# Performance work log

Measured on AMD Instinct MI355X. Metric: run time of the kernel, lower is better.

## Reference

```python
import jax, jax.numpy as jnp
import numpy as np
from jax import lax

DEPTH = 8
LEAK = 0.01  # activations.relu(x, 0.01) == leaky relu


def _lrelu(z):
    return jnp.where(z >= 0, z, LEAK * z)


def _forward(x, mask, bucket_size, W_emb, b_emb, W, U, b, W1, b1,
             W_action_1, U_action_1, b_action_1, W_action_3, b_action_3):
    S = int(bucket_size)
    B = x.shape[0]
    H = W_emb.shape[1]
    dm = mask.T[:S]                         # [S,B] data mask (float)
    xe = x @ W_emb + b_emb                  # [B,S,H] embedding
    xe = jnp.transpose(xe, (1, 0, 2))[:S]   # [S,B,H] time-major
    # last_value_mask: 1 only at the final time step
    lvm = jnp.concatenate([jnp.zeros((S - 1, B), jnp.float32),
                           jnp.ones((1, B), jnp.float32)], axis=0)

    def hstep(carry, seq):
        h_tm1, nm_tm1, hv_tm1 = carry
        xt, pm, phv, lv = seq
        # action MLP -> per-sample gate
        a = _lrelu(xt @ W_action_1 + h_tm1 @ U_action_1 + b_action_1)  # [B,A]
        nm = jnp.clip(0.2 * (a @ W_action_3 + b_action_3) + 0.5, 0.0, 1.0)[:, 0]  # hard_sigmoid
        nm = (1.0 - lv) * (pm * phv * nm)
        both = pm * phv * (1.0 - nm) * hv_tm1
        x_only = pm * phv * (nm + (1.0 - nm) * (1.0 - hv_tm1))
        h_only = (1.0 - pm + pm * (1.0 - phv)) * (1.0 - nm) * hv_tm1
        hv = both + x_only + h_only
        h_ = _lrelu(xt @ W + h_tm1 @ U + b)      # [B,inner]
        h_ = _lrelu(h_ @ W1 + b1)                # [B,H]
        h = both[:, None] * h_ + x_only[:, None] * xt + h_only[:, None] * h_tm1
        return (h, nm, hv), (h, nm, hv)

    def vstep(carry, _):
        xv, xm, phv = carry  # [S,B,H], [S,B], [S,B]
        init = (jnp.zeros((B, H), jnp.float32),
                jnp.ones((B,), jnp.float32),
                jnp.zeros((B,), jnp.float32))
        _, (hs, nms, hvs) = lax.scan(hstep, init, (xv, xm, phv, lvm))
        # shift new_mask left by one step, pad last step with ones
        nms = jnp.concatenate([nms[1:], jnp.ones((1, B), jnp.float32)], axis=0)
        return (hs, nms, hvs), None

    (hfin, _, _), _ = lax.scan(vstep, (xe, dm, dm), None, length=DEPTH - 1)
    return hfin[-1]  # [B,H]: last time step of the last vertical level


def setup_inputs() -> dict:
    key = jax.random.key(0)
    ks = jax.random.split(key, 9)
    B, S, IN, H, INNER, A = 64, 256, 256, 256, 512, 64
    g = lambda k, shp: jax.random.normal(k, shp, jnp.float32) * np.float32(np.sqrt(2.0 / (shp[0] + shp[1])))
    return {
        "x": jax.random.normal(ks[0], (B, S, IN), jnp.float32),
        "mask": jnp.ones((B, S), jnp.float32),
        "bucket_size": S,
        "W_emb": g(ks[1], (IN, H)),
        "b_emb": jnp.zeros((H,), jnp.float32),
        "W": g(ks[2], (H, INNER)),
        "U": g(ks[3], (H, INNER)),
        "b": jnp.zeros((INNER,), jnp.float32),
        "W1": g(ks[4], (INNER, H)),
        "b1": jnp.zeros((H,), jnp.float32),
        "W_action_1": g(ks[5], (H, A)),
        "U_action_1": g(ks[6], (H, A)),
        "b_action_1": jnp.zeros((A,), jnp.float32),
        "W_action_3": g(ks[7], (A, 1)),
        "b_action_3": jnp.zeros((1,), jnp.float32),
    }


def reference(x, mask, bucket_size, W_emb, b_emb, W, U, b, W1, b1,
              W_action_1, U_action_1, b_action_1, W_action_3, b_action_3):
    return _forward(x, mask, bucket_size, W_emb, b_emb, W, U, b, W1, b1,
                    W_action_1, U_action_1, b_action_1, W_action_3, b_action_3)
```

## Files before the change

### kernel.cpp

```cpp
#include <hip/hip_runtime.h>
#include <stdint.h>


typedef _Float16 f16x8 __attribute__((ext_vector_type(8)));
typedef float    f32x4 __attribute__((ext_vector_type(4)));

static constexpr int SS = 256, BB = 64, DIN = 256, DH = 256, DNN = 512, DA = 64;

static constexpr size_t OFF_FLAGS = 0;
static constexpr size_t OFF_WEMB  = 8192;
static constexpr size_t SZ_WEMB   = (size_t)DIN * DH * 2;
static constexpr size_t OFF_W     = OFF_WEMB + SZ_WEMB;
static constexpr size_t SZ_WU     = (size_t)DH * DNN * 2;
static constexpr size_t OFF_U     = OFF_W + SZ_WU;
static constexpr size_t OFF_W1    = OFF_U + SZ_WU;
static constexpr size_t SZ_W1     = (size_t)DNN * DH * 2;
static constexpr size_t OFF_WA1   = OFF_W1 + SZ_W1;
static constexpr size_t SZ_WA     = (size_t)DH * DA * 2;
static constexpr size_t OFF_UA1   = OFF_WA1 + SZ_WA;
static constexpr size_t OFF_NM    = OFF_UA1 + SZ_WA;
static constexpr size_t SZ_NM     = (size_t)SS * BB * 4;
static constexpr size_t OFF_HV    = OFF_NM + 8 * SZ_NM;
static constexpr size_t OFF_G1    = OFF_HV + 8 * SZ_NM;
static constexpr size_t SZ_G1     = (size_t)BB * DNN * 2;
static constexpr size_t OFF_Z     = OFF_G1 + 8 * SZ_G1;
static constexpr size_t OFF_HB    = (size_t)4 << 20;
static constexpr size_t SZ_HB     = (size_t)SS * BB * DH * 2;
static constexpr size_t WS_NEEDED = OFF_HB + 8 * SZ_HB;

__device__ __forceinline__ float lrelu(float v) { return v >= 0.0f ? v : 0.01f * v; }

__device__ __forceinline__ float gldf(const float* p) {
  return __hip_atomic_load((float*)p, __ATOMIC_RELAXED, __HIP_MEMORY_SCOPE_AGENT);
}
__device__ __forceinline__ void gstf(float* p, float v) {
  __hip_atomic_store(p, v, __ATOMIC_RELAXED, __HIP_MEMORY_SCOPE_AGENT);
}
__device__ __forceinline__ void gsth(_Float16* p, _Float16 v) {
  __hip_atomic_store(p, v, __ATOMIC_RELAXED, __HIP_MEMORY_SCOPE_AGENT);
}
__device__ __forceinline__ unsigned long long gld64(const _Float16* p) {
  return __hip_atomic_load((const unsigned long long*)p, __ATOMIC_RELAXED,
                           __HIP_MEMORY_SCOPE_AGENT);
}

__device__ __forceinline__ void poll8(unsigned* base, unsigned need) {
  for (int g = 0; g < (1 << 18); ++g) {
    unsigned mn = ~0u;
    #pragma unroll
    for (int p = 0; p < 8; ++p) {
      unsigned v = __hip_atomic_load(base + p, __ATOMIC_RELAXED, __HIP_MEMORY_SCOPE_AGENT);
      mn = v < mn ? v : mn;
    }
    if (mn >= need) return;
    __builtin_amdgcn_s_sleep(1);
  }
}

__global__ void zero_flags_k(unsigned* f) {
  f[threadIdx.x] = 0u;
  f[threadIdx.x + 1024] = 0u;
}

__global__ void pack_weight_k(const float* __restrict__ src, _Float16* __restrict__ dst,
                              int K, int N) {
  int idx = blockIdx.x * 256 + threadIdx.x;
  if (idx >= K * N) return;
  int k = idx / N, n = idx - k * N;
  int kt = k >> 5, q = (k >> 3) & 3, jj = k & 7;
  int nt = n >> 4, l = n & 15;
  size_t p = (((size_t)(kt * (N >> 4) + nt) * 4 + q) * 16 + l) * 8 + jj;
  dst[p] = (_Float16)src[idx];
}

__global__ __launch_bounds__(512, 2) void emb_k(const float* __restrict__ xin,
                                                const float* __restrict__ b_emb,
                                                char* __restrict__ ws) {
  const int tid = threadIdx.x, wave = tid >> 6, lane = tid & 63;
  const int l15 = lane & 15, quad = lane >> 4;
  const _Float16* Wp = (const _Float16*)(ws + OFF_WEMB);
  _Float16* xe = (_Float16*)(ws + OFF_HB);

  f16x8 bE[16];
  #pragma unroll
  for (int kt = 0; kt < 8; ++kt)
    #pragma unroll
    for (int i = 0; i < 2; ++i)
      bE[kt * 2 + i] = *(const f16x8*)(Wp + (((size_t)(kt * 16 + (wave * 2 + i)) * 4 + quad) * 16 + l15) * 8);
  float ber[2] = { b_emb[(wave * 2) * 16 + l15], b_emb[(wave * 2 + 1) * 16 + l15] };

  __shared__ _Float16 xtF[32 * 65 * 8];

  for (int tt = 0; tt < 4; ++tt) {
    const int t = (int)blockIdx.x + 64 * tt;
    #pragma unroll
    for (int c = 0; c < 4; ++c) {
      int u = tid + 512 * c;
      int s = u >> 5, kg = u & 31;
      const float* src = xin + ((size_t)s * SS + t) * DIN + kg * 8;
      f32x4 v0 = *(const f32x4*)src, v1 = *(const f32x4*)(src + 4);
      f16x8 p;
      p[0]=(_Float16)v0[0]; p[1]=(_Float16)v0[1]; p[2]=(_Float16)v0[2]; p[3]=(_Float16)v0[3];
      p[4]=(_Float16)v1[0]; p[5]=(_Float16)v1[1]; p[6]=(_Float16)v1[2]; p[7]=(_Float16)v1[3];
      *(f16x8*)(xtF + ((size_t)kg * 65 + s) * 8) = p;
    }
    __syncthreads();
    f32x4 acc[2][4] = {};
    #pragma unroll
    for (int kt = 0; kt < 8; ++kt) {
      f16x8 ax[4];
      #pragma unroll
      for (int mt = 0; mt < 4; ++mt)
        ax[mt] = *(const f16x8*)(xtF + (((size_t)(kt * 4 + quad)) * 65 + (mt * 16 + l15)) * 8);
      #pragma unroll
      for (int i = 0; i < 2; ++i)
        #pragma unroll
        for (int mt = 0; mt < 4; ++mt)
          acc[i][mt] = __builtin_amdgcn_mfma_f32_16x16x32_f16(ax[mt], bE[kt * 2 + i], acc[i][mt], 0, 0, 0);
    }
    #pragma unroll
    for (int i = 0; i < 2; ++i) {
      int n = (wave * 2 + i) * 16 + l15;
      #pragma unroll
      for (int mt = 0; mt < 4; ++mt)
        #pragma unroll
        for (int r = 0; r < 4; ++r) {
          int s = mt * 16 + quad * 4 + r;
          gsth(&xe[((size_t)t * BB + s) * DH + n], (_Float16)(acc[i][mt][r] + ber[i]));
        }
    }
    __syncthreads();
  }
}

__global__ __launch_bounds__(512, 2) void pipe_k(
    const float* __restrict__ mask, const float* __restrict__ b_in,
    const float* __restrict__ b1v, const float* __restrict__ bA1,
    const float* __restrict__ WA3, const float* __restrict__ bA3,
    char* __restrict__ ws, float* __restrict__ outp) {
  const int level = 1 + ((int)blockIdx.x >> 3);
  const int j     = (int)blockIdx.x & 7;
  const int tid   = threadIdx.x, wave = tid >> 6, lane = tid & 63;
  const int l15   = lane & 15, quad = lane >> 4;

  unsigned* flags = (unsigned*)(ws + OFF_FLAGS);
  unsigned* hfl   = flags + level * 64;
  unsigned* hflP  = flags + (level - 1) * 64;
  unsigned* gfl   = flags + (8 + level) * 64;

  const _Float16* Wp   = (const _Float16*)(ws + OFF_W);
  const _Float16* Up   = (const _Float16*)(ws + OFF_U);
  const _Float16* W1p  = (const _Float16*)(ws + OFF_W1);
  const _Float16* WA1p = (const _Float16*)(ws + OFF_WA1);
  const _Float16* UA1p = (const _Float16*)(ws + OFF_UA1);

  const _Float16* xsrc = (const _Float16*)(ws + OFF_HB) + (size_t)(level - 1) * SS * BB * DH;
  _Float16*       hdst = (_Float16*)(ws + OFF_HB) + (size_t)level * SS * BB * DH;
  _Float16*       g1b  = (_Float16*)(ws + OFF_G1 + (size_t)level * SZ_G1);
  float*          zb   = (float*)(ws + OFF_Z + (size_t)level * 4096);
  float*          nmW  = (float*)(ws + OFF_NM + (size_t)level * SZ_NM);
  float*          hvW  = (float*)(ws + OFF_HV + (size_t)level * SZ_NM);
  const float*    nmR  = (const float*)(ws + OFF_NM + (size_t)(level - 1) * SZ_NM);
  const float*    hvR  = (const float*)(ws + OFF_HV + (size_t)(level - 1) * SZ_NM);

  const int ntG = j * 4 + (wave >> 1);
  const int m0  = (wave & 1) * 2;
  f16x8 bW[8], bU[8];
  #pragma unroll
  for (int kt = 0; kt < 8; ++kt) {
    bW[kt] = *(const f16x8*)(Wp + (((size_t)(kt * 32 + ntG) * 4 + quad) * 16 + l15) * 8);
    bU[kt] = *(const f16x8*)(Up + (((size_t)(kt * 32 + ntG) * 4 + quad) * 16 + l15) * 8);
  }
  const int nt1 = j * 2 + (wave & 1);
  const int mt1 = wave >> 1;
  f16x8 b1f[16];
  #pragma unroll
  for (int kt = 0; kt < 16; ++kt)
    b1f[kt] = *(const f16x8*)(W1p + (((size_t)(kt * 16 + nt1) * 4 + quad) * 16 + l15) * 8);

  const int nG = ntG * 16 + l15;
  const int nC = nt1 * 16 + l15;
  const float bir = b_in[nG];
  const float b1r = b1v[nC];
  const float wa3r = WA3[(j & 3) * 16 + l15];
  const float ba1r = bA1[(j & 3) * 16 + l15];
  const float bA3v = bA3[0];

  __shared__ _Float16 xtF[32 * 65 * 8];
  __shared__ _Float16 htF[32 * 65 * 8];
  __shared__ _Float16 g1F[64 * 65 * 8];
  __shared__ _Float16 waF[16 * 64 * 8];
  __shared__ float gB[64], gX[64], gH[64], gHv[64];

  if (j < 4) {
    for (int u = tid; u < 1024; u += 512) {
      int ktm = u >> 6, lu = u & 63, kt = ktm >> 1, m = ktm & 1;
      const _Float16* sp = (m ? UA1p : WA1p) +
          (((size_t)(kt * 4 + j) * 4 + (lu >> 4)) * 16 + (lu & 15)) * 8;
      *(f16x8*)(waF + (size_t)u * 8) = *(const f16x8*)sp;
    }
  }
  for (int i = tid; i < 32 * 65 * 8; i += 512) htF[i] = (_Float16)0;
  if (tid < 64) gHv[tid] = 0.0f;
  float hreg[4] = {0.f, 0.f, 0.f, 0.f};
  __syncthreads();

  for (int t = 0; t < SS; ++t) {
    if (tid == 0) {
      if (t > 0) poll8(hfl, (unsigned)t);
      if (level >= 2) {
        unsigned need = (unsigned)((t + 2 <= SS) ? (t + 2) : SS);
        poll8(hflP, need);
      }
    }
    __syncthreads();

    {
      const _Float16* xp = xsrc + (size_t)t * BB * DH;
      #pragma unroll
      for (int c = 0; c < 4; ++c) {
        int u = tid + 512 * c, s = u >> 5, kq = u & 31;
        const _Float16* p = xp + s * DH + kq * 8;
        unsigned long long lo = gld64(p), hi = gld64(p + 4);
        unsigned long long* d = (unsigned long long*)(xtF + ((size_t)kq * 65 + s) * 8);
        d[0] = lo; d[1] = hi;
      }
      if (t > 0) {
        const _Float16* hp = hdst + (size_t)(t - 1) * BB * DH;
        #pragma unroll
        for (int c = 0; c < 4; ++c) {
          int u = tid + 512 * c, s = u >> 5, kq = u & 31;
          const _Float16* p = hp + s * DH + kq * 8;
          unsigned long long lo = gld64(p), hi = gld64(p + 4);
          unsigned long long* d = (unsigned long long*)(htF + ((size_t)kq * 65 + s) * 8);
          d[0] = lo; d[1] = hi;
        }
      }
    }
    __syncthreads();

    {
      f32x4 a0 = {}, a1 = {};
      #pragma unroll
      for (int kt = 0; kt < 8; ++kt) {
        int kq = kt * 4 + quad;
        f16x8 ax0 = *(const f16x8*)(xtF + ((size_t)kq * 65 + (m0 * 16 + l15)) * 8);
        f16x8 ax1 = *(const f16x8*)(xtF + ((size_t)kq * 65 + ((m0 + 1) * 16 + l15)) * 8);
        f16x8 ah0 = *(const f16x8*)(htF + ((size_t)kq * 65 + (m0 * 16 + l15)) * 8);
        f16x8 ah1 = *(const f16x8*)(htF + ((size_t)kq * 65 + ((m0 + 1) * 16 + l15)) * 8);
        a0 = __builtin_amdgcn_mfma_f32_16x16x32_f16(ax0, bW[kt], a0, 0, 0, 0);
        a1 = __builtin_amdgcn_mfma_f32_16x16x32_f16(ax1, bW[kt], a1, 0, 0, 0);
        a0 = __builtin_amdgcn_mfma_f32_16x16x32_f16(ah0, bU[kt], a0, 0, 0, 0);
        a1 = __builtin_amdgcn_mfma_f32_16x16x32_f16(ah1, bU[kt], a1, 0, 0, 0);
      }
      #pragma unroll
      for (int r = 0; r < 4; ++r) {
        gsth(&g1b[(size_t)(m0 * 16 + quad * 4 + r) * DNN + nG], (_Float16)lrelu(a0[r] + bir));
        gsth(&g1b[(size_t)((m0 + 1) * 16 + quad * 4 + r) * DNN + nG], (_Float16)lrelu(a1[r] + bir));
      }
    }
    if (j < 4 && wave < 4) {
      f32x4 aa = {};
      #pragma unroll
      for (int kt = 0; kt < 8; ++kt) {
        int kq = kt * 4 + quad;
        f16x8 ax = *(const f16x8*)(xtF + ((size_t)kq * 65 + (wave * 16 + l15)) * 8);
        f16x8 ah = *(const f16x8*)(htF + ((size_t)kq * 65 + (wave * 16 + l15)) * 8);
        f16x8 bWa = *(const f16x8*)(waF + ((size_t)(kt * 2) * 64 + lane) * 8);
        f16x8 bUa = *(const f16x8*)(waF + ((size_t)(kt * 2 + 1) * 64 + lane) * 8);
        aa = __builtin_amdgcn_mfma_f32_16x16x32_f16(ax, bWa, aa, 0, 0, 0);
        aa = __builtin_amdgcn_mfma_f32_16x16x32_f16(ah, bUa, aa, 0, 0, 0);
      }
      #pragma unroll
      for (int r = 0; r < 4; ++r) {
        float v = lrelu(aa[r] + ba1r) * wa3r;
        v += __shfl_xor(v, 1); v += __shfl_xor(v, 2);
        v += __shfl_xor(v, 4); v += __shfl_xor(v, 8);
        if (l15 == 0) gstf(&zb[j * 64 + wave * 16 + quad * 4 + r], v);
      }
    }
    __syncthreads();
    if (tid == 0)
      __hip_atomic_store(gfl + j, (unsigned)(t + 1), __ATOMIC_RELEASE, __HIP_MEMORY_SCOPE_AGENT);

    if (tid == 0) poll8(gfl, (unsigned)(t + 1));
    __syncthreads();

    #pragma unroll
    for (int c = 0; c < 8; ++c) {
      int u = tid + 512 * c, s = u >> 6, kq = u & 63;
      const _Float16* p = g1b + (size_t)s * DNN + kq * 8;
      unsigned long long lo = gld64(p), hi = gld64(p + 4);
      unsigned long long* d = (unsigned long long*)(g1F + ((size_t)kq * 65 + s) * 8);
      d[0] = lo; d[1] = hi;
    }
    if (tid < 64) {
      int s = tid;
      float z = bA3v + gldf(&zb[s]) + gldf(&zb[64 + s]) + gldf(&zb[128 + s]) + gldf(&zb[192 + s]);
      float nm0 = fminf(fmaxf(0.2f * z + 0.5f, 0.0f), 1.0f);
      float pm, phv;
      if (level == 1) {
        float mv = mask[(size_t)s * SS + t];
        pm = mv; phv = mv;
      } else {
        pm  = (t + 1 < SS) ? gldf(&nmR[(size_t)(t + 1) * BB + s]) : 1.0f;
        phv = gldf(&hvR[(size_t)t * BB + s]);
      }
      float lv   = (t == SS - 1) ? 1.0f : 0.0f;
      float nm   = (1.0f - lv) * (pm * phv * nm0);
      float hvp  = gHv[s], omn = 1.0f - nm;
      float both = pm * phv * omn * hvp;
      float xo   = pm * phv * (nm + omn * (1.0f - hvp));
      float ho   = (1.0f - pm * phv) * omn * hvp;
      float hv   = both + xo + ho;
      gB[s] = both; gX[s] = xo; gH[s] = ho; gHv[s] = hv;
      if (j == 0 && level < 7) {
        gstf(&nmW[(size_t)t * BB + s], nm);
        gstf(&hvW[(size_t)t * BB + s], hv);
      }
    }
    __syncthreads();

    {
      f32x4 c1 = {};
      #pragma unroll
      for (int kt = 0; kt < 16; ++kt) {
        f16x8 ag = *(const f16x8*)(g1F + ((size_t)(kt * 4 + quad) * 65 + (mt1 * 16 + l15)) * 8);
        c1 = __builtin_amdgcn_mfma_f32_16x16x32_f16(ag, b1f[kt], c1, 0, 0, 0);
      }
      const int kqc = nC >> 3, sub = nC & 7;
      #pragma unroll
      for (int r = 0; r < 4; ++r) {
        int s = mt1 * 16 + quad * 4 + r;
        float h1  = lrelu(c1[r] + b1r);
        float xtv = (float)xtF[((size_t)kqc * 65 + s) * 8 + sub];
        float hn  = gB[s] * h1 + gX[s] * xtv + gH[s] * hreg[r];
        hreg[r] = hn;
        gsth(&hdst[((size_t)t * BB + s) * DH + nC], (_Float16)hn);
        if (level == 7 && t == SS - 1) outp[(size_t)s * DH + nC] = hn;
      }
    }
    __syncthreads();
    if (tid == 0)
      __hip_atomic_store(hfl + j, (unsigned)(t + 1), __ATOMIC_RELEASE, __HIP_MEMORY_SCOPE_AGENT);
  }
}

extern "C" void kernel_launch(void* const* d_in, const int* in_sizes, int n_in,
                              void* d_out, int out_size, void* d_ws, size_t ws_size,
                              hipStream_t stream) {
  const float* x     = (const float*)d_in[0];
  const float* mask  = (const float*)d_in[1];
  const float* W_emb = (const float*)d_in[3];
  const float* b_emb = (const float*)d_in[4];
  const float* W     = (const float*)d_in[5];
  const float* U     = (const float*)d_in[6];
  const float* b     = (const float*)d_in[7];
  const float* W1    = (const float*)d_in[8];
  const float* b1    = (const float*)d_in[9];
  const float* WA1   = (const float*)d_in[10];
  const float* UA1   = (const float*)d_in[11];
  const float* bA1   = (const float*)d_in[12];
  const float* WA3   = (const float*)d_in[13];
  const float* bA3   = (const float*)d_in[14];
  char* ws = (char*)d_ws;

  if (ws_size < WS_NEEDED) return;

  zero_flags_k<<<1, 1024, 0, stream>>>((unsigned*)(ws + OFF_FLAGS));
  pack_weight_k<<<(DIN * DH + 255) / 256, 256, 0, stream>>>(W_emb, (_Float16*)(ws + OFF_WEMB), DIN, DH);
  pack_weight_k<<<(DH * DNN + 255) / 256, 256, 0, stream>>>(W, (_Float16*)(ws + OFF_W), DH, DNN);
  pack_weight_k<<<(DH * DNN + 255) / 256, 256, 0, stream>>>(U, (_Float16*)(ws + OFF_U), DH, DNN);
  pack_weight_k<<<(DNN * DH + 255) / 256, 256, 0, stream>>>(W1, (_Float16*)(ws + OFF_W1), DNN, DH);
  pack_weight_k<<<(DH * DA + 255) / 256, 256, 0, stream>>>(WA1, (_Float16*)(ws + OFF_WA1), DH, DA);
  pack_weight_k<<<(DH * DA + 255) / 256, 256, 0, stream>>>(UA1, (_Float16*)(ws + OFF_UA1), DH, DA);

  emb_k<<<64, 512, 0, stream>>>(x, b_emb, ws);
  pipe_k<<<56, 512, 0, stream>>>(mask, b, b1, bA1, WA3, bA3, ws, (float*)d_out);
}
```

Before: 3.877 ms.

## Restructure cross-block exchange with tiled layout, per-wave polling and prefetch

Stores hidden states and g1 activations in the MFMA-tiled layout so each block exchanges them with coalesced 128-bit loads and stores that use cache-bypass bits, instead of scattered 16-bit atomics. Each wave now polls only the flag of the peer block whose slice it copies, and the block skips copying its own slice because it is already in shared memory. The next step's x input is prefetched during the g1 exchange, and the second GEMM starts before the gate computation finishes. The change adds inline-asm memory ordering with explicit vmcnt waits, which can break visibility between blocks if a wait or fence is missing.

```diff
diff --git a/kernel.cpp b/kernel.cpp
--- a/kernel.cpp
+++ b/kernel.cpp
@@ -30,30 +30,31 @@
 
 __device__ __forceinline__ float lrelu(float v) { return v >= 0.0f ? v : 0.01f * v; }
 
-__device__ __forceinline__ float gldf(const float* p) {
-  return __hip_atomic_load((float*)p, __ATOMIC_RELAXED, __HIP_MEMORY_SCOPE_AGENT);
-}
-__device__ __forceinline__ void gstf(float* p, float v) {
-  __hip_atomic_store(p, v, __ATOMIC_RELAXED, __HIP_MEMORY_SCOPE_AGENT);
-}
-__device__ __forceinline__ void gsth(_Float16* p, _Float16 v) {
-  __hip_atomic_store(p, v, __ATOMIC_RELAXED, __HIP_MEMORY_SCOPE_AGENT);
-}
-__device__ __forceinline__ unsigned long long gld64(const _Float16* p) {
-  return __hip_atomic_load((const unsigned long long*)p, __ATOMIC_RELAXED,
-                           __HIP_MEMORY_SCOPE_AGENT);
-}
-
-__device__ __forceinline__ void poll8(unsigned* base, unsigned need) {
+__device__ __forceinline__ f32x4 ld128(const f32x4* p) {
+  f32x4 r;
+  asm volatile("global_load_dwordx4 %0, %1, off sc0 sc1" : "=v"(r) : "v"(p) : "memory");
+  return r;
+}
+__device__ __forceinline__ void st128(f32x4* p, f32x4 v) {
+  asm volatile("global_store_dwordx4 %0, %1, off sc0 sc1" :: "v"(p), "v"(v) : "memory");
+}
+__device__ __forceinline__ float ldf(const float* p) {
+  float r;
+  asm volatile("global_load_dword %0, %1, off sc0 sc1" : "=v"(r) : "v"(p) : "memory");
+  return r;
+}
+__device__ __forceinline__ void stf(float* p, float v) {
+  asm volatile("global_store_dword %0, %1, off sc0 sc1" :: "v"(p), "v"(v) : "memory");
+}
+__device__ __forceinline__ void vwait() { asm volatile("s_waitcnt vmcnt(0)" ::: "memory"); }
+
+__device__ __forceinline__ void pollf(const unsigned* p, unsigned need) {
+  #pragma nounroll
   for (int g = 0; g < (1 << 18); ++g) {
-    unsigned mn = ~0u;
-    #pragma unroll
-    for (int p = 0; p < 8; ++p) {
-      unsigned v = __hip_atomic_load(base + p, __ATOMIC_RELAXED, __HIP_MEMORY_SCOPE_AGENT);
-      mn = v < mn ? v : mn;
-    }
-    if (mn >= need) return;
-    __builtin_amdgcn_s_sleep(1);
+    unsigned v;
+    asm volatile("global_load_dword %0, %1, off sc0 sc1\n\ts_waitcnt vmcnt(0)"
+                 : "=v"(v) : "v"(p) : "memory");
+    if (v >= need) return;
   }
 }
 
@@ -89,14 +90,14 @@
       bE[kt * 2 + i] = *(const f16x8*)(Wp + (((size_t)(kt * 16 + (wave * 2 + i)) * 4 + quad) * 16 + l15) * 8);
   float ber[2] = { b_emb[(wave * 2) * 16 + l15], b_emb[(wave * 2 + 1) * 16 + l15] };
 
-  __shared__ _Float16 xtF[32 * 65 * 8];
+  __shared__ __align__(16) _Float16 xtF[32 * 65 * 8];
+  __shared__ __align__(16) _Float16 oF[32 * 65 * 8];
 
   for (int tt = 0; tt < 4; ++tt) {
     const int t = (int)blockIdx.x + 64 * tt;
     #pragma unroll
     for (int c = 0; c < 4; ++c) {
-      int u = tid + 512 * c;
-      int s = u >> 5, kg = u & 31;
+      int u = tid + 512 * c, s = u >> 5, kg = u & 31;
       const float* src = xin + ((size_t)s * SS + t) * DIN + kg * 8;
       f32x4 v0 = *(const f32x4*)src, v1 = *(const f32x4*)(src + 4);
       f16x8 p;
@@ -121,13 +122,21 @@
     #pragma unroll
     for (int i = 0; i < 2; ++i) {
       int n = (wave * 2 + i) * 16 + l15;
+      int kq = n >> 3, jn = n & 7;
       #pragma unroll
       for (int mt = 0; mt < 4; ++mt)
         #pragma unroll
         for (int r = 0; r < 4; ++r) {
           int s = mt * 16 + quad * 4 + r;
-          gsth(&xe[((size_t)t * BB + s) * DH + n], (_Float16)(acc[i][mt][r] + ber[i]));
+          oF[((size_t)kq * 65 + s) * 8 + jn] = (_Float16)(acc[i][mt][r] + ber[i]);
         }
+    }
+    __syncthreads();
+    #pragma unroll
+    for (int c = 0; c < 4; ++c) {
+      int u = tid + 512 * c, kq = u >> 6, s = u & 63;
+      f32x4 v = *(const f32x4*)(oF + ((size_t)kq * 65 + s) * 8);
+      *((f32x4*)(xe + (((size_t)t * 32 + kq) * 64 + s) * 8)) = v;
     }
     __syncthreads();
   }
@@ -154,14 +163,14 @@
   const _Float16* WA1p = (const _Float16*)(ws + OFF_WA1);
   const _Float16* UA1p = (const _Float16*)(ws + OFF_UA1);
 
-  const _Float16* xsrc = (const _Float16*)(ws + OFF_HB) + (size_t)(level - 1) * SS * BB * DH;
-  _Float16*       hdst = (_Float16*)(ws + OFF_HB) + (size_t)level * SS * BB * DH;
-  _Float16*       g1b  = (_Float16*)(ws + OFF_G1 + (size_t)level * SZ_G1);
-  float*          zb   = (float*)(ws + OFF_Z + (size_t)level * 4096);
-  float*          nmW  = (float*)(ws + OFF_NM + (size_t)level * SZ_NM);
-  float*          hvW  = (float*)(ws + OFF_HV + (size_t)level * SZ_NM);
-  const float*    nmR  = (const float*)(ws + OFF_NM + (size_t)(level - 1) * SZ_NM);
-  const float*    hvR  = (const float*)(ws + OFF_HV + (size_t)(level - 1) * SZ_NM);
+  const f32x4* hPrev4 = (const f32x4*)((_Float16*)(ws + OFF_HB) + (size_t)(level - 1) * SS * BB * DH);
+  f32x4*       hOwn4  = (f32x4*)((_Float16*)(ws + OFF_HB) + (size_t)level * SS * BB * DH);
+  f32x4*       g1g4   = (f32x4*)(ws + OFF_G1 + (size_t)level * SZ_G1);
+  float*       zg     = (float*)(ws + OFF_Z + (size_t)level * 4096);
+  float*       nmW    = (float*)(ws + OFF_NM + (size_t)level * SZ_NM);
+  float*       hvW    = (float*)(ws + OFF_HV + (size_t)level * SZ_NM);
+  const float* nmR    = (const float*)(ws + OFF_NM + (size_t)(level - 1) * SZ_NM);
+  const float* hvR    = (const float*)(ws + OFF_HV + (size_t)(level - 1) * SZ_NM);
 
   const int ntG = j * 4 + (wave >> 1);
   const int m0  = (wave & 1) * 2;
@@ -180,16 +189,16 @@
 
   const int nG = ntG * 16 + l15;
   const int nC = nt1 * 16 + l15;
-  const float bir = b_in[nG];
-  const float b1r = b1v[nC];
+  const float bir  = b_in[nG];
+  const float b1r  = b1v[nC];
   const float wa3r = WA3[(j & 3) * 16 + l15];
   const float ba1r = bA1[(j & 3) * 16 + l15];
   const float bA3v = bA3[0];
 
-  __shared__ _Float16 xtF[32 * 65 * 8];
-  __shared__ _Float16 htF[32 * 65 * 8];
-  __shared__ _Float16 g1F[64 * 65 * 8];
-  __shared__ _Float16 waF[16 * 64 * 8];
+  __shared__ __align__(16) _Float16 xtF[32 * 64 * 8];
+  __shared__ __align__(16) _Float16 htF[32 * 64 * 8];
+  __shared__ __align__(16) _Float16 g1F[64 * 64 * 8];
+  __shared__ __align__(16) _Float16 waF[16 * 64 * 8];
   __shared__ float gB[64], gX[64], gH[64], gHv[64];
 
   if (j < 4) {
@@ -200,42 +209,39 @@
       *(f16x8*)(waF + (size_t)u * 8) = *(const f16x8*)sp;
     }
   }
-  for (int i = tid; i < 32 * 65 * 8; i += 512) htF[i] = (_Float16)0;
+  for (int i = tid; i < 32 * 64 * 8; i += 512) htF[i] = (_Float16)0;
   if (tid < 64) gHv[tid] = 0.0f;
   float hreg[4] = {0.f, 0.f, 0.f, 0.f};
   __syncthreads();
 
+  if (level >= 2) pollf(hflP + wave, 1);
+  __syncthreads();
+  {
+    f32x4 pf[4];
+    #pragma unroll
+    for (int c = 0; c < 4; ++c) pf[c] = ld128(hPrev4 + tid + 512 * c);
+    vwait();
+    #pragma unroll
+    for (int c = 0; c < 4; ++c) ((f32x4*)xtF)[tid + 512 * c] = pf[c];
+  }
+  __syncthreads();
+
   for (int t = 0; t < SS; ++t) {
-    if (tid == 0) {
-      if (t > 0) poll8(hfl, (unsigned)t);
-      if (level >= 2) {
-        unsigned need = (unsigned)((t + 2 <= SS) ? (t + 2) : SS);
-        poll8(hflP, need);
-      }
-    }
-    __syncthreads();
-
-    {
-      const _Float16* xp = xsrc + (size_t)t * BB * DH;
-      #pragma unroll
-      for (int c = 0; c < 4; ++c) {
-        int u = tid + 512 * c, s = u >> 5, kq = u & 31;
-        const _Float16* p = xp + s * DH + kq * 8;
-        unsigned long long lo = gld64(p), hi = gld64(p + 4);
-        unsigned long long* d = (unsigned long long*)(xtF + ((size_t)kq * 65 + s) * 8);
-        d[0] = lo; d[1] = hi;
-      }
-      if (t > 0) {
-        const _Float16* hp = hdst + (size_t)(t - 1) * BB * DH;
-        #pragma unroll
-        for (int c = 0; c < 4; ++c) {
-          int u = tid + 512 * c, s = u >> 5, kq = u & 31;
-          const _Float16* p = hp + s * DH + kq * 8;
-          unsigned long long lo = gld64(p), hi = gld64(p + 4);
-          unsigned long long* d = (unsigned long long*)(htF + ((size_t)kq * 65 + s) * 8);
-          d[0] = lo; d[1] = hi;
-        }
-      }
+    const bool last = (t == SS - 1);
+
+    if (t > 0) pollf(hfl + wave, (unsigned)t);
+    if (level >= 2) {
+      unsigned need = (unsigned)((t + 2 <= SS) ? (t + 2) : SS);
+      pollf(hflP + wave, need);
+    }
+    if (t > 0 && wave != j) {
+      const f32x4* src = hOwn4 + (size_t)(t - 1) * 2048 + wave * 256;
+      f32x4 hv4[4];
+      #pragma unroll
+      for (int it = 0; it < 4; ++it) hv4[it] = ld128(src + it * 64 + lane);
+      vwait();
+      #pragma unroll
+      for (int it = 0; it < 4; ++it) ((f32x4*)htF)[wave * 256 + it * 64 + lane] = hv4[it];
     }
     __syncthreads();
 
@@ -244,69 +250,91 @@
       #pragma unroll
       for (int kt = 0; kt < 8; ++kt) {
         int kq = kt * 4 + quad;
-        f16x8 ax0 = *(const f16x8*)(xtF + ((size_t)kq * 65 + (m0 * 16 + l15)) * 8);
-        f16x8 ax1 = *(const f16x8*)(xtF + ((size_t)kq * 65 + ((m0 + 1) * 16 + l15)) * 8);
-        f16x8 ah0 = *(const f16x8*)(htF + ((size_t)kq * 65 + (m0 * 16 + l15)) * 8);
-        f16x8 ah1 = *(const f16x8*)(htF + ((size_t)kq * 65 + ((m0 + 1) * 16 + l15)) * 8);
+        f16x8 ax0 = *(const f16x8*)(xtF + ((size_t)(kq * 64 + m0 * 16 + l15)) * 8);
+        f16x8 ax1 = *(const f16x8*)(xtF + ((size_t)(kq * 64 + (m0 + 1) * 16 + l15)) * 8);
+        f16x8 ah0 = *(const f16x8*)(htF + ((size_t)(kq * 64 + m0 * 16 + l15)) * 8);
+        f16x8 ah1 = *(const f16x8*)(htF + ((size_t)(kq * 64 + (m0 + 1) * 16 + l15)) * 8);
         a0 = __builtin_amdgcn_mfma_f32_16x16x32_f16(ax0, bW[kt], a0, 0, 0, 0);
         a1 = __builtin_amdgcn_mfma_f32_16x16x32_f16(ax1, bW[kt], a1, 0, 0, 0);
         a0 = __builtin_amdgcn_mfma_f32_16x16x32_f16(ah0, bU[kt], a0, 0, 0, 0);
         a1 = __builtin_amdgcn_mfma_f32_16x16x32_f16(ah1, bU[kt], a1, 0, 0, 0);
       }
+      const int kqn = nG >> 3, jn = nG & 7;
       #pragma unroll
       for (int r = 0; r < 4; ++r) {
-        gsth(&g1b[(size_t)(m0 * 16 + quad * 4 + r) * DNN + nG], (_Float16)lrelu(a0[r] + bir));
-        gsth(&g1b[(size_t)((m0 + 1) * 16 + quad * 4 + r) * DNN + nG], (_Float16)lrelu(a1[r] + bir));
-      }
-    }
-    if (j < 4 && wave < 4) {
-      f32x4 aa = {};
-      #pragma unroll
-      for (int kt = 0; kt < 8; ++kt) {
-        int kq = kt * 4 + quad;
-        f16x8 ax = *(const f16x8*)(xtF + ((size_t)kq * 65 + (wave * 16 + l15)) * 8);
-        f16x8 ah = *(const f16x8*)(htF + ((size_t)kq * 65 + (wave * 16 + l15)) * 8);
-        f16x8 bWa = *(const f16x8*)(waF + ((size_t)(kt * 2) * 64 + lane) * 8);
-        f16x8 bUa = *(const f16x8*)(waF + ((size_t)(kt * 2 + 1) * 64 + lane) * 8);
-        aa = __builtin_amdgcn_mfma_f32_16x16x32_f16(ax, bWa, aa, 0, 0, 0);
-        aa = __builtin_amdgcn_mfma_f32_16x16x32_f16(ah, bUa, aa, 0, 0, 0);
-      }
-      #pragma unroll
-      for (int r = 0; r < 4; ++r) {
-        float v = lrelu(aa[r] + ba1r) * wa3r;
-        v += __shfl_xor(v, 1); v += __shfl_xor(v, 2);
-        v += __shfl_xor(v, 4); v += __shfl_xor(v, 8);
-        if (l15 == 0) gstf(&zb[j * 64 + wave * 16 + quad * 4 + r], v);
-      }
+        g1F[((size_t)kqn * 64 + (m0 * 16 + quad * 4 + r)) * 8 + jn]       = (_Float16)lrelu(a0[r] + bir);
+        g1F[((size_t)kqn * 64 + ((m0 + 1) * 16 + quad * 4 + r)) * 8 + jn] = (_Float16)lrelu(a1[r] + bir);
+      }
+      if (j < 4 && wave < 4) {
+        f32x4 aa = {};
+        #pragma unroll
+        for (int kt = 0; kt < 8; ++kt) {
+          int kq = kt * 4 + quad;
+          f16x8 ax = *(const f16x8*)(xtF + ((size_t)(kq * 64 + wave * 16 + l15)) * 8);
+          f16x8 ah = *(const f16x8*)(htF + ((size_t)(kq * 64 + wave * 16 + l15)) * 8);
+          f16x8 bWa = *(const f16x8*)(waF + ((size_t)(kt * 2) * 64 + lane) * 8);
+          f16x8 bUa = *(const f16x8*)(waF + ((size_t)(kt * 2 + 1) * 64 + lane) * 8);
+          aa = __builtin_amdgcn_mfma_f32_16x16x32_f16(ax, bWa, aa, 0, 0, 0);
+          aa = __builtin_amdgcn_mfma_f32_16x16x32_f16(ah, bUa, aa, 0, 0, 0);
+        }
+        #pragma unroll
+        for (int r = 0; r < 4; ++r) {
+          float v = lrelu(aa[r] + ba1r) * wa3r;
+          v += __shfl_xor(v, 1); v += __shfl_xor(v, 2);
+          v += __shfl_xor(v, 4); v += __shfl_xor(v, 8);
+          if (l15 == 0) stf(&zg[j * 64 + wave * 16 + quad * 4 + r], v);
+        }
+      }
+    }
+    __syncthreads();
+    {
+      f32x4 v = ((const f32x4*)g1F)[j * 512 + tid];
+      st128(g1g4 + j * 512 + tid, v);
+      vwait();
     }
     __syncthreads();
     if (tid == 0)
       __hip_atomic_store(gfl + j, (unsigned)(t + 1), __ATOMIC_RELEASE, __HIP_MEMORY_SCOPE_AGENT);
 
-    if (tid == 0) poll8(gfl, (unsigned)(t + 1));
-    __syncthreads();
-
-    #pragma unroll
-    for (int c = 0; c < 8; ++c) {
-      int u = tid + 512 * c, s = u >> 6, kq = u & 63;
-      const _Float16* p = g1b + (size_t)s * DNN + kq * 8;
-      unsigned long long lo = gld64(p), hi = gld64(p + 4);
-      unsigned long long* d = (unsigned long long*)(g1F + ((size_t)kq * 65 + s) * 8);
-      d[0] = lo; d[1] = hi;
-    }
+    f32x4 pf[4];
+    if (!last) {
+      const f32x4* xs = hPrev4 + (size_t)(t + 1) * 2048;
+      #pragma unroll
+      for (int c = 0; c < 4; ++c) pf[c] = ld128(xs + tid + 512 * c);
+      vwait();
+    }
+
+    if (wave != j) {
+      pollf(gfl + wave, (unsigned)(t + 1));
+      const f32x4* src = g1g4 + wave * 512;
+      f32x4 g4[8];
+      #pragma unroll
+      for (int it = 0; it < 8; ++it) g4[it] = ld128(src + it * 64 + lane);
+      vwait();
+      #pragma unroll
+      for (int it = 0; it < 8; ++it) ((f32x4*)g1F)[wave * 512 + it * 64 + lane] = g4[it];
+    }
+    __syncthreads();
+
     if (tid < 64) {
       int s = tid;
-      float z = bA3v + gldf(&zb[s]) + gldf(&zb[64 + s]) + gldf(&zb[128 + s]) + gldf(&zb[192 + s]);
-      float nm0 = fminf(fmaxf(0.2f * z + 0.5f, 0.0f), 1.0f);
+      float z0 = ldf(zg + s), z1 = ldf(zg + 64 + s), z2 = ldf(zg + 128 + s), z3 = ldf(zg + 192 + s);
       float pm, phv;
       if (level == 1) {
+        vwait();
         float mv = mask[(size_t)s * SS + t];
         pm = mv; phv = mv;
       } else {
-        pm  = (t + 1 < SS) ? gldf(&nmR[(size_t)(t + 1) * BB + s]) : 1.0f;
-        phv = gldf(&hvR[(size_t)t * BB + s]);
-      }
-      float lv   = (t == SS - 1) ? 1.0f : 0.0f;
+        size_t tn = (t + 1 < SS) ? (size_t)(t + 1) : 0;
+        float pmv = ldf(nmR + tn * BB + s);
+        float ph  = ldf(hvR + (size_t)t * BB + s);
+        vwait();
+        pm  = (t + 1 < SS) ? pmv : 1.0f;
+        phv = ph;
+      }
+      float z    = bA3v + z0 + z1 + z2 + z3;
+      float nm0  = fminf(fmaxf(0.2f * z + 0.5f, 0.0f), 1.0f);
+      float lv   = last ? 1.0f : 0.0f;
       float nm   = (1.0f - lv) * (pm * phv * nm0);
       float hvp  = gHv[s], omn = 1.0f - nm;
       float both = pm * phv * omn * hvp;
@@ -315,31 +343,41 @@
       float hv   = both + xo + ho;
       gB[s] = both; gX[s] = xo; gH[s] = ho; gHv[s] = hv;
       if (j == 0 && level < 7) {
-        gstf(&nmW[(size_t)t * BB + s], nm);
-        gstf(&hvW[(size_t)t * BB + s], hv);
-      }
+        stf(&nmW[(size_t)t * BB + s], nm);
+        stf(&hvW[(size_t)t * BB + s], hv);
+      }
+    }
+    f32x4 c1 = {};
+    #pragma unroll
+    for (int kt = 0; kt < 16; ++kt) {
+      f16x8 ag = *(const f16x8*)(g1F + ((size_t)((kt * 4 + quad) * 64 + mt1 * 16 + l15)) * 8);
+      c1 = __builtin_amdgcn_mfma_f32_16x16x32_f16(ag, b1f[kt], c1, 0, 0, 0);
     }
     __syncthreads();
 
     {
-      f32x4 c1 = {};
-      #pragma unroll
-      for (int kt = 0; kt < 16; ++kt) {
-        f16x8 ag = *(const f16x8*)(g1F + ((size_t)(kt * 4 + quad) * 65 + (mt1 * 16 + l15)) * 8);
-        c1 = __builtin_amdgcn_mfma_f32_16x16x32_f16(ag, b1f[kt], c1, 0, 0, 0);
-      }
-      const int kqc = nC >> 3, sub = nC & 7;
+      const int kqc = nC >> 3, jc = nC & 7;
       #pragma unroll
       for (int r = 0; r < 4; ++r) {
         int s = mt1 * 16 + quad * 4 + r;
         float h1  = lrelu(c1[r] + b1r);
-        float xtv = (float)xtF[((size_t)kqc * 65 + s) * 8 + sub];
+        float xtv = (float)xtF[((size_t)(kqc * 64 + s)) * 8 + jc];
         float hn  = gB[s] * h1 + gX[s] * xtv + gH[s] * hreg[r];
         hreg[r] = hn;
-        gsth(&hdst[((size_t)t * BB + s) * DH + nC], (_Float16)hn);
-        if (level == 7 && t == SS - 1) outp[(size_t)s * DH + nC] = hn;
-      }
-    }
+        htF[((size_t)(kqc * 64 + s)) * 8 + jc] = (_Float16)hn;
+        if (level == 7 && last) outp[(size_t)s * DH + nC] = hn;
+      }
+    }
+    __syncthreads();
+    if (tid < 256) {
+      f32x4 v = ((const f32x4*)htF)[j * 256 + tid];
+      st128(hOwn4 + (size_t)t * 2048 + j * 256 + tid, v);
+    }
+    if (!last) {
+      #pragma unroll
+      for (int c = 0; c < 4; ++c) ((f32x4*)xtF)[tid + 512 * c] = pf[c];
+    }
+    vwait();
     __syncthreads();
     if (tid == 0)
       __hip_atomic_store(hfl + j, (unsigned)(t + 1), __ATOMIC_RELEASE, __HIP_MEMORY_SCOPE_AGENT);
```

New measurement: 3.598 ms. 1.08x faster.
